# Optimization experiments

Hardware: AMD Instinct MI355X
Metric: run time of the kernel (lower is better)

Reference implementation:

```python
import jax, jax.numpy as jnp
import numpy as np

N = 131072   # total inner-graph nodes (G * n)
G = 2048     # number of inner graphs = nodes of outer graph fg
n = 64       # nodes per inner graph (contiguous blocks)
E = 1048576  # inner edges
EF = 32768   # outer (fg) edges
D = 128      # emb_dim == hidden_dim
K = 8        # SortPooling k
VOCAB = 150


def setup_inputs() -> dict:
    key = jax.random.key(0)
    ks = jax.random.split(key, 32)
    p = lambda k, shape: (jax.random.normal(k, shape, jnp.float32) * 0.1)
    inp = {
        'h': jax.random.randint(ks[0], (N,), 0, VOCAB),
        'g_src': jax.random.randint(ks[1], (E,), 0, N),
        'g_dst': jax.random.randint(ks[2], (E,), 0, N),
        'fg_src': jax.random.randint(ks[3], (EF,), 0, G),
        'fg_dst': jax.random.randint(ks[4], (EF,), 0, G),
        'token_emb': p(ks[5], (VOCAB, D)),
        # GATConv 1 (D -> D, 1 head): fc weight (in,out), attn vectors, output bias
        'W1': p(ks[6], (D, D)), 'al1': p(ks[7], (D,)), 'ar1': p(ks[8], (D,)), 'b1': p(ks[9], (D,)),
        # GATConv 2
        'W2': p(ks[10], (D, D)), 'al2': p(ks[11], (D,)), 'ar2': p(ks[12], (D,)), 'b2': p(ks[13], (D,)),
        # GATConv 3 (K*D -> D) over fg
        'W3': p(ks[14], (K * D, D)), 'al3': p(ks[15], (D,)), 'ar3': p(ks[16], (D,)), 'b3': p(ks[17], (D,)),
        # linear_forward
        'Wf': p(ks[18], (D, D)), 'bf': p(ks[19], (D,)),
        # linear
        'Wl': p(ks[20], (D, D)), 'bl': p(ks[21], (D,)),
        # linear1
        'Wl1': p(ks[22], (D, D)), 'bl1': p(ks[23], (D,)),
        # clasifier
        'Wc': p(ks[24], (D, 2)), 'bc': p(ks[25], (2,)),
    }
    return inp


def gat_conv(src, dst, num_nodes, x, W, al, ar, b):
    """DGL GATConv, num_heads=1, allow_zero_in_degree=True, no activation."""
    f = x @ W                                   # [N, D] projected features
    el = f @ al                                 # [N] left attention logits
    er = f @ ar                                 # [N] right attention logits
    e = jax.nn.leaky_relu(el[src] + er[dst], 0.2)   # [E] per-edge score
    m = jax.ops.segment_max(e, dst, num_segments=num_nodes)
    a = jnp.exp(e - m[dst])
    s = jax.ops.segment_sum(a, dst, num_segments=num_nodes)
    alpha = a / s[dst]                          # edge softmax over incoming edges
    out = jax.ops.segment_sum(alpha[:, None] * f[src], dst, num_segments=num_nodes)
    return out + b                              # zero-in-degree nodes -> bias only


def sort_pooling(x, num_graphs, nodes_per_graph, k):
    """DGL SortPooling: sort each node's feature ascending, rank nodes by last
    channel descending, take top-k, concat -> [G, k*D]."""
    d = x.shape[-1]
    x = jnp.sort(x.reshape(num_graphs, nodes_per_graph, d), axis=-1)
    idx = jnp.argsort(-x[:, :, -1], axis=1)[:, :k]          # [G, k]
    topk = jnp.take_along_axis(x, idx[:, :, None], axis=1)  # [G, k, D]
    return topk.reshape(num_graphs, k * d)


def reference(h, g_src, g_dst, fg_src, fg_dst, token_emb,
              W1, al1, ar1, b1, W2, al2, ar2, b2, W3, al3, ar3, b3,
              Wf, bf, Wl, bl, Wl1, bl1, Wc, bc):
    x = jax.nn.relu(token_emb[h])                                   # [N, D]
    x = jax.nn.relu(gat_conv(g_src, g_dst, N, x, W1, al1, ar1, b1))
    x = jax.nn.relu(gat_conv(g_src, g_dst, N, x, W2, al2, ar2, b2))
    x = jax.nn.relu(x @ Wf + bf)                                    # linear_forward
    x = sort_pooling(x, G, n, K)                                    # [G, K*D]
    x = jax.nn.relu(gat_conv(fg_src, fg_dst, G, x, W3, al3, ar3, b3))
    x = jax.nn.relu(x @ Wl + bl)                                    # dropout = eval identity
    x = jax.nn.relu(x @ Wl1 + bl1)
    x = x @ Wc + bc
    return x.reshape(-1, 2)
```

## Files before the change

kernel.cpp:

```cpp
#include <hip/hip_runtime.h>
#include <math.h>

#define NN   131072
#define GG   2048
#define NPG  64
#define EE   1048576
#define EFN  32768
#define DD   128
#define KK   8

typedef unsigned short bfu;
typedef _Float16 f16x8 __attribute__((ext_vector_type(8)));
typedef float f32x4 __attribute__((ext_vector_type(4)));

static __device__ __forceinline__ bfu f2b(float f) {
  unsigned u = __float_as_uint(f);
  u += 0x7FFFu + ((u >> 16) & 1u);
  return (bfu)(u >> 16);
}
static __device__ __forceinline__ float b2f(bfu b) {
  return __uint_as_float(((unsigned)b) << 16);
}

static __device__ __forceinline__ bfu f2h(float f) {
  _Float16 h = (_Float16)f;
  bfu u;
  __builtin_memcpy(&u, &h, 2);
  return u;
}
static __device__ __forceinline__ float h2f(bfu b) {
  _Float16 h;
  __builtin_memcpy(&h, &b, 2);
  return (float)h;
}

__global__ void fill_f32_kernel(float* __restrict__ p, float v, int nElems) {
  int i = blockIdx.x * 256 + threadIdx.x;
  if (i < nElems) p[i] = v;
}

__global__ void zero_int_kernel(int* __restrict__ p, int nElems) {
  int i = blockIdx.x * 256 + threadIdx.x;
  if (i < nElems) p[i] = 0;
}

__global__ void init_softmax_kernel(float* __restrict__ mx, float* __restrict__ sm, int nElems) {
  int i = blockIdx.x * 256 + threadIdx.x;
  if (i < nElems) { mx[i] = -INFINITY; sm[i] = 0.f; }
}

__global__ void embed_relu_kernel(const float* __restrict__ temb,
                                  const int* __restrict__ h,
                                  float* __restrict__ x, int total) {
  int i = blockIdx.x * 256 + threadIdx.x;
  if (i >= total) return;
  int node = i >> 7, d = i & 127;
  x[i] = fmaxf(temb[h[node] * DD + d], 0.f);
}

template <int KD, int ROWS>
__global__ __launch_bounds__(128) void gemm_kernel(
    const float* __restrict__ A, const float* __restrict__ W,
    const float* __restrict__ bias, float* __restrict__ out,
    int relu_flag) {
  __shared__ float As[ROWS * KD];
  const int row0 = blockIdx.x * ROWS;
  const int tid = threadIdx.x;
  for (int i = tid; i < ROWS * KD; i += 128) As[i] = A[(size_t)row0 * KD + i];
  __syncthreads();
  float acc[ROWS];
#pragma unroll
  for (int r = 0; r < ROWS; r++) acc[r] = 0.f;
  for (int k = 0; k < KD; k++) {
    float w = W[k * 128 + tid];
#pragma unroll
    for (int r = 0; r < ROWS; r++) acc[r] += As[r * KD + k] * w;
  }
  float b = bias ? bias[tid] : 0.f;
#pragma unroll
  for (int r = 0; r < ROWS; r++) {
    float v = acc[r] + b;
    if (relu_flag) v = fmaxf(v, 0.f);
    out[(size_t)(row0 + r) * 128 + tid] = v;
  }
}

__global__ __launch_bounds__(256) void gemm1024_kernel(
    const float* __restrict__ A, const float* __restrict__ W,
    float* __restrict__ out) {
  __shared__ float As[8 * 1024];
  __shared__ float red[8][256];
  const int t = threadIdx.x;
  const int row0 = blockIdx.x * 8;
  for (int idx = t; idx < 8 * 256; idx += 256) {
    int r = idx >> 8, c4 = (idx & 255) << 2;
    *(float4*)&As[r * 1024 + c4] = *(const float4*)(A + (size_t)(row0 + r) * 1024 + c4);
  }
  __syncthreads();
  const int col = t & 127, kh = t >> 7;
  const int k0 = kh * 512;
  float acc[8];
#pragma unroll
  for (int r = 0; r < 8; r++) acc[r] = 0.f;
  for (int k = k0; k < k0 + 512; k += 4) {
    float w0 = W[(size_t)(k + 0) * 128 + col];
    float w1 = W[(size_t)(k + 1) * 128 + col];
    float w2 = W[(size_t)(k + 2) * 128 + col];
    float w3 = W[(size_t)(k + 3) * 128 + col];
#pragma unroll
    for (int r = 0; r < 8; r++) {
      float4 a = *(const float4*)&As[r * 1024 + k];
      acc[r] += a.x * w0 + a.y * w1 + a.z * w2 + a.w * w3;
    }
  }
#pragma unroll
  for (int r = 0; r < 8; r++) red[r][t] = acc[r];
  __syncthreads();
  for (int idx = t; idx < 1024; idx += 256) {
    int r = idx >> 7, c = idx & 127;
    out[(size_t)(row0 + r) * 128 + c] = red[r][c] + red[r][128 + c];
  }
}

__global__ void pack_w_kernel(const float* __restrict__ W,
                              bfu* __restrict__ hi) {
  int i = blockIdx.x * 256 + threadIdx.x;
  if (i >= 16384) return;
  int k = i >> 7, n = i & 127;
  bfu h = f2h(W[i]);
  int kk = k >> 5, k5 = k & 31, quad = k5 >> 3, j = k5 & 7;
  int tt = n >> 4, m16 = n & 15;
  int pos = ((((kk * 8 + tt) * 4 + quad) * 16) + m16) * 8 + j;
  hi[pos] = h;
}

template <int SRC_MODE, int EPI>
__global__ __launch_bounds__(256) void mfma_gemm(
    const float* A, const float* __restrict__ temb,
    const int* __restrict__ hidx,
    const bfu* __restrict__ WfHi,
    const float* __restrict__ bias, void* out,
    const float* __restrict__ al, const float* __restrict__ ar,
    float* __restrict__ el, float* __restrict__ er,
    float* __restrict__ keyb) {
  const int t = threadIdx.x;
  const int lane = t & 63, wv_ = t >> 6;
  const int m16 = lane & 15, quad = lane >> 4;
  const int rowbase = blockIdx.x * 128 + wv_ * 32;
  const float* arow0 = nullptr;
  const float* arow1 = nullptr;
  const bfu* brow0 = nullptr;
  const bfu* brow1 = nullptr;
  if constexpr (SRC_MODE == 1) {
    arow0 = temb + (size_t)hidx[rowbase + m16] * 128;
    arow1 = temb + (size_t)hidx[rowbase + 16 + m16] * 128;
  } else if constexpr (SRC_MODE == 0) {
    arow0 = A + (size_t)(rowbase + m16) * 128;
    arow1 = A + (size_t)(rowbase + 16 + m16) * 128;
  } else {
    brow0 = (const bfu*)A + (size_t)(rowbase + m16) * 128;
    brow1 = (const bfu*)A + (size_t)(rowbase + 16 + m16) * 128;
  }
  f32x4 acc[2][8];
#pragma unroll
  for (int rg = 0; rg < 2; rg++)
#pragma unroll
    for (int i = 0; i < 8; i++) acc[rg][i] = (f32x4){0.f, 0.f, 0.f, 0.f};
#pragma unroll
  for (int kk = 0; kk < 4; kk++) {
    int k0 = kk * 32 + quad * 8;
    f16x8 ahi0, alo0, ahi1, alo1;
    if constexpr (SRC_MODE == 2) {
      ahi0 = *(const f16x8*)(brow0 + k0);
      ahi1 = *(const f16x8*)(brow1 + k0);
    } else {
      float av0[8], av1[8];
      *(float4*)&av0[0] = *(const float4*)(arow0 + k0);
      *(float4*)&av0[4] = *(const float4*)(arow0 + k0 + 4);
      *(float4*)&av1[0] = *(const float4*)(arow1 + k0);
      *(float4*)&av1[4] = *(const float4*)(arow1 + k0 + 4);
      if (SRC_MODE == 1) {
#pragma unroll
        for (int i = 0; i < 8; i++) {
          av0[i] = fmaxf(av0[i], 0.f);
          av1[i] = fmaxf(av1[i], 0.f);
        }
      }
#pragma unroll
      for (int i = 0; i < 8; i++) {
        _Float16 h0 = (_Float16)av0[i];
        ahi0[i] = h0;
        alo0[i] = (_Float16)(av0[i] - (float)h0);
        _Float16 h1 = (_Float16)av1[i];
        ahi1[i] = h1;
        alo1[i] = (_Float16)(av1[i] - (float)h1);
      }
    }
#pragma unroll
    for (int tt = 0; tt < 8; tt++) {
      int pos = ((((kk * 8 + tt) * 4 + quad) * 16) + m16) * 8;
      f16x8 bhi = *(const f16x8*)&WfHi[pos];
      acc[0][tt] = __builtin_amdgcn_mfma_f32_16x16x32_f16(ahi0, bhi, acc[0][tt], 0, 0, 0);
      if constexpr (SRC_MODE != 2)
        acc[0][tt] = __builtin_amdgcn_mfma_f32_16x16x32_f16(alo0, bhi, acc[0][tt], 0, 0, 0);
      acc[1][tt] = __builtin_amdgcn_mfma_f32_16x16x32_f16(ahi1, bhi, acc[1][tt], 0, 0, 0);
      if constexpr (SRC_MODE != 2)
        acc[1][tt] = __builtin_amdgcn_mfma_f32_16x16x32_f16(alo1, bhi, acc[1][tt], 0, 0, 0);
    }
  }
#pragma unroll
  for (int rg = 0; rg < 2; rg++) {
    const int rb = rowbase + rg * 16;
    if constexpr (EPI == 1) {
      float pl[4] = {0.f, 0.f, 0.f, 0.f}, pr[4] = {0.f, 0.f, 0.f, 0.f};
#pragma unroll
      for (int tt = 0; tt < 8; tt++) {
        int col = tt * 16 + m16;
        float alv = al[col], arv = ar[col];
#pragma unroll
        for (int r = 0; r < 4; r++) {
          float v = acc[rg][tt][r];
          ((bfu*)out)[(size_t)(rb + quad * 4 + r) * 128 + col] = f2h(v);
          pl[r] += v * alv;
          pr[r] += v * arv;
        }
      }
#pragma unroll
      for (int r = 0; r < 4; r++) {
        float a0 = pl[r], a1 = pr[r];
#pragma unroll
        for (int off = 1; off < 16; off <<= 1) {
          a0 += __shfl_xor(a0, off);
          a1 += __shfl_xor(a1, off);
        }
        if (m16 == 0) {
          el[rb + quad * 4 + r] = a0;
          er[rb + quad * 4 + r] = a1;
        }
      }
    } else {
      float pm[4] = {-INFINITY, -INFINITY, -INFINITY, -INFINITY};
#pragma unroll
      for (int tt = 0; tt < 8; tt++) {
        int col = tt * 16 + m16;
        float bv = bias[col];
#pragma unroll
        for (int r = 0; r < 4; r++) {
          float v = fmaxf(acc[rg][tt][r] + bv, 0.f);
          ((bfu*)out)[(size_t)(rb + quad * 4 + r) * 128 + col] = f2h(v);
          pm[r] = fmaxf(pm[r], v);
        }
      }
#pragma unroll
      for (int r = 0; r < 4; r++) {
        float a0 = pm[r];
#pragma unroll
        for (int off = 1; off < 16; off <<= 1) a0 = fmaxf(a0, __shfl_xor(a0, off));
        if (m16 == 0) keyb[rb + quad * 4 + r] = a0;
      }
    }
  }
}

__global__ __launch_bounds__(64) void attn_logits_kernel(
    const float* __restrict__ f, const float* __restrict__ al,
    const float* __restrict__ ar, float* __restrict__ el,
    float* __restrict__ er) {
  int node = blockIdx.x, lane = threadIdx.x;
  float v1 = f[(size_t)node * 128 + lane];
  float v2 = f[(size_t)node * 128 + 64 + lane];
  float sl = v1 * al[lane] + v2 * al[64 + lane];
  float sr = v1 * ar[lane] + v2 * ar[64 + lane];
#pragma unroll
  for (int off = 32; off; off >>= 1) {
    sl += __shfl_down(sl, off);
    sr += __shfl_down(sr, off);
  }
  if (lane == 0) { el[node] = sl; er[node] = sr; }
}

__global__ void hist_rank_kernel(const int* __restrict__ dst, int* __restrict__ cnt,
                                 int* __restrict__ rank, int nE) {
  int e = blockIdx.x * 256 + threadIdx.x;
  if (e < nE) rank[e] = atomicAdd(&cnt[dst[e]], 1);
}

__global__ __launch_bounds__(256) void scan_block_kernel(
    const int* __restrict__ cnt, int* __restrict__ excl, int* __restrict__ part) {
  __shared__ int s[256];
  int blk = blockIdx.x, tid = threadIdx.x;
  int base = blk * 1024 + tid * 4;
  int a0 = cnt[base], a1 = cnt[base + 1], a2 = cnt[base + 2], a3 = cnt[base + 3];
  int tsum = a0 + a1 + a2 + a3;
  s[tid] = tsum; __syncthreads();
  for (int off = 1; off < 256; off <<= 1) {
    int v = (tid >= off) ? s[tid - off] : 0;
    __syncthreads();
    s[tid] += v;
    __syncthreads();
  }
  int texcl = s[tid] - tsum;
  excl[base]     = texcl;
  excl[base + 1] = texcl + a0;
  excl[base + 2] = texcl + a0 + a1;
  excl[base + 3] = texcl + a0 + a1 + a2;
  if (tid == 255) part[blk] = s[255];
}

__global__ __launch_bounds__(128) void scan_part_kernel(int* __restrict__ part) {
  __shared__ int s[128];
  int tid = threadIdx.x;
  int orig = part[tid];
  s[tid] = orig; __syncthreads();
  for (int off = 1; off < 128; off <<= 1) {
    int v = (tid >= off) ? s[tid - off] : 0;
    __syncthreads();
    s[tid] += v;
    __syncthreads();
  }
  part[tid] = s[tid] - orig;
}

__global__ void scan_add_kernel(int* __restrict__ row_ptr, const int* __restrict__ part,
                                int n, int total) {
  int i = blockIdx.x * 256 + threadIdx.x;
  if (i < n) row_ptr[i] += part[i >> 10];
  if (i == 0) row_ptr[n] = total;
}

__global__ __launch_bounds__(256) void scan2048_kernel(const int* __restrict__ cnt,
                                                       int* __restrict__ rp, int total) {
  __shared__ int s[256];
  int t = threadIdx.x;
  int base = t * 8;
  int v[8];
  int tsum = 0;
#pragma unroll
  for (int i = 0; i < 8; i++) { v[i] = cnt[base + i]; tsum += v[i]; }
  s[t] = tsum; __syncthreads();
  for (int off = 1; off < 256; off <<= 1) {
    int x = (t >= off) ? s[t - off] : 0;
    __syncthreads();
    s[t] += x;
    __syncthreads();
  }
  int excl = s[t] - tsum;
#pragma unroll
  for (int i = 0; i < 8; i++) { rp[base + i] = excl; excl += v[i]; }
  if (t == 255) rp[2048] = total;
}

__global__ void scatter2_kernel(const int* __restrict__ dst, const int* __restrict__ src,
                                const int* __restrict__ row_ptr, const int* __restrict__ rank,
                                int* __restrict__ adj_src, int nE) {
  int e = blockIdx.x * 256 + threadIdx.x;
  if (e >= nE) return;
  adj_src[row_ptr[dst[e]] + rank[e]] = src[e];
}

__global__ __launch_bounds__(256) void gat_aggregate_csr_kernel(
    const bfu* __restrict__ F, const float* __restrict__ el,
    const float* __restrict__ er, const int* __restrict__ row_ptr,
    const int* __restrict__ adj_src,
    const float* __restrict__ bias, bfu* __restrict__ outX) {
  const int t = threadIdx.x;
  const int l = t & 31;
  const int gb = t & 32;
  const int d = blockIdx.x * 8 + (t >> 5);
  const int c0 = l * 4;
  int beg = row_ptr[d];
  int n = row_ptr[d + 1] - beg;
  float4 bv = *(const float4*)&bias[c0];
  if (n == 0) {
    ushort4 o;
    o.x = f2h(fmaxf(bv.x, 0.f)); o.y = f2h(fmaxf(bv.y, 0.f));
    o.z = f2h(fmaxf(bv.z, 0.f)); o.w = f2h(fmaxf(bv.w, 0.f));
    *(ushort4*)&outX[(size_t)d * 128 + c0] = o;
    return;
  }
  float er_d = er[d];
  float4 acc = make_float4(0.f, 0.f, 0.f, 0.f);
  if (n <= 32) {
    int sv = 0; float sc = -INFINITY;
    if (l < n) {
      sv = adj_src[beg + l];
      float v = el[sv] + er_d;
      sc = v > 0.f ? v : 0.2f * v;
    }
    float m = sc;
#pragma unroll
    for (int off = 16; off; off >>= 1) m = fmaxf(m, __shfl_xor(m, off));
    float ex = (l < n) ? expf(sc - m) : 0.f;
    float s = ex;
#pragma unroll
    for (int off = 16; off; off >>= 1) s += __shfl_xor(s, off);
    float wt = ex / s;
    for (int j = 0; j < n; j += 4) {
      int   s0 = __shfl(sv, gb + j);
      float w0 = __shfl(wt, gb + j);
      int   j1 = (j + 1 < n) ? j + 1 : j;
      int   s1 = __shfl(sv, gb + j1); float w1 = (j + 1 < n) ? __shfl(wt, gb + j1) : 0.f;
      int   j2 = (j + 2 < n) ? j + 2 : j;
      int   s2 = __shfl(sv, gb + j2); float w2 = (j + 2 < n) ? __shfl(wt, gb + j2) : 0.f;
      int   j3 = (j + 3 < n) ? j + 3 : j;
      int   s3 = __shfl(sv, gb + j3); float w3 = (j + 3 < n) ? __shfl(wt, gb + j3) : 0.f;
      ushort4 f0 = *(const ushort4*)&F[(size_t)s0 * 128 + c0];
      ushort4 f1 = *(const ushort4*)&F[(size_t)s1 * 128 + c0];
      ushort4 f2 = *(const ushort4*)&F[(size_t)s2 * 128 + c0];
      ushort4 f3 = *(const ushort4*)&F[(size_t)s3 * 128 + c0];
      acc.x += w0 * h2f(f0.x) + w1 * h2f(f1.x) + w2 * h2f(f2.x) + w3 * h2f(f3.x);
      acc.y += w0 * h2f(f0.y) + w1 * h2f(f1.y) + w2 * h2f(f2.y) + w3 * h2f(f3.y);
      acc.z += w0 * h2f(f0.z) + w1 * h2f(f1.z) + w2 * h2f(f2.z) + w3 * h2f(f3.z);
      acc.w += w0 * h2f(f0.w) + w1 * h2f(f1.w) + w2 * h2f(f2.w) + w3 * h2f(f3.w);
    }
  } else {
    float lm = -INFINITY;
    for (int e = l; e < n; e += 32) {
      int sv = adj_src[beg + e];
      float v = el[sv] + er_d;
      v = v > 0.f ? v : 0.2f * v;
      lm = fmaxf(lm, v);
    }
#pragma unroll
    for (int off = 16; off; off >>= 1) lm = fmaxf(lm, __shfl_xor(lm, off));
    float ls = 0.f;
    for (int e = l; e < n; e += 32) {
      int sv = adj_src[beg + e];
      float v = el[sv] + er_d;
      v = v > 0.f ? v : 0.2f * v;
      ls += expf(v - lm);
    }
#pragma unroll
    for (int off = 16; off; off >>= 1) ls += __shfl_xor(ls, off);
    for (int base = 0; base < n; base += 32) {
      int e = base + l;
      int sv = 0; float wt = 0.f;
      if (e < n) {
        sv = adj_src[beg + e];
        float v = el[sv] + er_d;
        v = v > 0.f ? v : 0.2f * v;
        wt = expf(v - lm) / ls;
      }
      int cnt = min(32, n - base);
      for (int j = 0; j < cnt; ++j) {
        int s0 = __shfl(sv, gb + j);
        float w0 = __shfl(wt, gb + j);
        ushort4 f0 = *(const ushort4*)&F[(size_t)s0 * 128 + c0];
        acc.x += w0 * h2f(f0.x);
        acc.y += w0 * h2f(f0.y);
        acc.z += w0 * h2f(f0.z);
        acc.w += w0 * h2f(f0.w);
      }
    }
  }
  ushort4 o;
  o.x = f2h(fmaxf(acc.x + bv.x, 0.f));
  o.y = f2h(fmaxf(acc.y + bv.y, 0.f));
  o.z = f2h(fmaxf(acc.z + bv.z, 0.f));
  o.w = f2h(fmaxf(acc.w + bv.w, 0.f));
  *(ushort4*)&outX[(size_t)d * 128 + c0] = o;
}

__global__ __launch_bounds__(256) void gat_aggregate_outer_kernel(
    const float* __restrict__ F, const float* __restrict__ el,
    const float* __restrict__ er, const int* __restrict__ row_ptr,
    const int* __restrict__ adj_src,
    const float* __restrict__ bias, float* __restrict__ outG) {
  const int t = threadIdx.x;
  const int l = t & 31;
  const int gb = t & 32;
  const int d = blockIdx.x * 8 + (t >> 5);
  const int c0 = l * 4;
  int beg = row_ptr[d];
  int n = row_ptr[d + 1] - beg;
  float4 bv = *(const float4*)&bias[c0];
  if (n == 0) {
    float4 o;
    o.x = fmaxf(bv.x, 0.f); o.y = fmaxf(bv.y, 0.f);
    o.z = fmaxf(bv.z, 0.f); o.w = fmaxf(bv.w, 0.f);
    *(float4*)&outG[(size_t)d * 128 + c0] = o;
    return;
  }
  float er_d = er[d];
  float4 acc = make_float4(0.f, 0.f, 0.f, 0.f);
  if (n <= 32) {
    int sv = 0; float sc = -INFINITY;
    if (l < n) {
      sv = adj_src[beg + l];
      float v = el[sv] + er_d;
      sc = v > 0.f ? v : 0.2f * v;
    }
    float m = sc;
#pragma unroll
    for (int off = 16; off; off >>= 1) m = fmaxf(m, __shfl_xor(m, off));
    float ex = (l < n) ? expf(sc - m) : 0.f;
    float s = ex;
#pragma unroll
    for (int off = 16; off; off >>= 1) s += __shfl_xor(s, off);
    float wt = ex / s;
    for (int j = 0; j < n; ++j) {
      int   s0 = __shfl(sv, gb + j);
      float w0 = __shfl(wt, gb + j);
      float4 f0 = *(const float4*)&F[(size_t)s0 * 128 + c0];
      acc.x += w0 * f0.x; acc.y += w0 * f0.y;
      acc.z += w0 * f0.z; acc.w += w0 * f0.w;
    }
  } else {
    float lm = -INFINITY;
    for (int e = l; e < n; e += 32) {
      int sv = adj_src[beg + e];
      float v = el[sv] + er_d;
      v = v > 0.f ? v : 0.2f * v;
      lm = fmaxf(lm, v);
    }
#pragma unroll
    for (int off = 16; off; off >>= 1) lm = fmaxf(lm, __shfl_xor(lm, off));
    float ls = 0.f;
    for (int e = l; e < n; e += 32) {
      int sv = adj_src[beg + e];
      float v = el[sv] + er_d;
      v = v > 0.f ? v : 0.2f * v;
      ls += expf(v - lm);
    }
#pragma unroll
    for (int off = 16; off; off >>= 1) ls += __shfl_xor(ls, off);
    for (int base = 0; base < n; base += 32) {
      int e = base + l;
      int sv = 0; float wt = 0.f;
      if (e < n) {
        sv = adj_src[beg + e];
        float v = el[sv] + er_d;
        v = v > 0.f ? v : 0.2f * v;
        wt = expf(v - lm) / ls;
      }
      int cnt = min(32, n - base);
      for (int j = 0; j < cnt; ++j) {
        int s0 = __shfl(sv, gb + j);
        float w0 = __shfl(wt, gb + j);
        float4 f0 = *(const float4*)&F[(size_t)s0 * 128 + c0];
        acc.x += w0 * f0.x; acc.y += w0 * f0.y;
        acc.z += w0 * f0.z; acc.w += w0 * f0.w;
      }
    }
  }
  float4 o;
  o.x = fmaxf(acc.x + bv.x, 0.f);
  o.y = fmaxf(acc.y + bv.y, 0.f);
  o.z = fmaxf(acc.z + bv.z, 0.f);
  o.w = fmaxf(acc.w + bv.w, 0.f);
  *(float4*)&outG[(size_t)d * 128 + c0] = o;
}

static __device__ __forceinline__ void atomicMaxF(float* addr, float v) {
  int iv = __float_as_int(v);
  if (iv >= 0) atomicMax((int*)addr, iv);
  else atomicMin((unsigned int*)addr, (unsigned int)iv);
}

static __device__ __forceinline__ float edge_score(const float* el, const float* er,
                                                   int sv, int dv) {
  float v = el[sv] + er[dv];
  return v > 0.f ? v : 0.2f * v;
}

__global__ void edge_max_kernel(const float* __restrict__ el,
                                const float* __restrict__ er,
                                const int* __restrict__ src,
                                const int* __restrict__ dst,
                                float* __restrict__ m, int nE) {
  int e = blockIdx.x * 256 + threadIdx.x;
  if (e >= nE) return;
  atomicMaxF(&m[dst[e]], edge_score(el, er, src[e], dst[e]));
}

__global__ void edge_expsum_kernel(const float* __restrict__ el,
                                   const float* __restrict__ er,
                                   const float* __restrict__ m,
                                   const int* __restrict__ src,
                                   const int* __restrict__ dst,
                                   float* __restrict__ s, int nE) {
  int e = blockIdx.x * 256 + threadIdx.x;
  if (e >= nE) return;
  int d = dst[e];
  atomicAdd(&s[d], expf(edge_score(el, er, src[e], d) - m[d]));
}

__global__ __launch_bounds__(128) void edge_aggregate_kernel(
    const float* __restrict__ f, const float* __restrict__ el,
    const float* __restrict__ er, const float* __restrict__ m,
    const float* __restrict__ s, const int* __restrict__ src,
    const int* __restrict__ dst, float* __restrict__ out, int nE) {
  int e = blockIdx.x;
  int d = threadIdx.x;
  int sv = src[e], dv = dst[e];
  float alpha = expf(edge_score(el, er, sv, dv) - m[dv]) / s[dv];
  atomicAdd(&out[(size_t)dv * 128 + d], alpha * f[(size_t)sv * 128 + d]);
}

__global__ void bias_relu_kernel(float* __restrict__ x,
                                 const float* __restrict__ b, int total) {
  int i = blockIdx.x * 256 + threadIdx.x;
  if (i >= total) return;
  x[i] = fmaxf(x[i] + b[i & 127], 0.f);
}

__global__ __launch_bounds__(64) void row_max_kernel(const float* __restrict__ x,
                                                     float* __restrict__ key) {
  int node = blockIdx.x, lane = threadIdx.x;
  float v = fmaxf(x[(size_t)node * 128 + lane], x[(size_t)node * 128 + 64 + lane]);
#pragma unroll
  for (int off = 32; off; off >>= 1) v = fmaxf(v, __shfl_down(v, off));
  if (lane == 0) key[node] = v;
}

__global__ __launch_bounds__(64) void select_topk_kernel(
    const float* __restrict__ key, int* __restrict__ sel) {
  __shared__ float keys[NPG];
  int g = blockIdx.x, t = threadIdx.x;
  keys[t] = key[(size_t)g * NPG + t];
  __syncthreads();
  float myk = keys[t];
  int rank = 0;
  for (int j = 0; j < NPG; ++j) {
    float kj = keys[j];
    rank += (kj > myk) || (kj == myk && j < t);
  }
  if (rank < KK) sel[g * KK + rank] = t;
}

template <int HF>
__global__ __launch_bounds__(128) void sort_rows_kernel(
    const void* __restrict__ xin, const int* __restrict__ sel,
    float* __restrict__ xp) {
  __shared__ float v[128];
  int b = blockIdx.x;
  int t = threadIdx.x;
  int g = b >> 3, r = b & 7;
  int node = sel[b];
  if (HF) v[t] = h2f(((const bfu*)xin)[(size_t)(g * NPG + node) * 128 + t]);
  else    v[t] = ((const float*)xin)[(size_t)(g * NPG + node) * 128 + t];
  __syncthreads();
  for (int k = 2; k <= 128; k <<= 1) {
    for (int j = k >> 1; j > 0; j >>= 1) {
      int ixj = t ^ j;
      if (ixj > t) {
        float a = v[t], bb = v[ixj];
        bool asc = ((t & k) == 0);
        if (asc ? (a > bb) : (a < bb)) { v[t] = bb; v[ixj] = a; }
      }
      __syncthreads();
    }
  }
  xp[(size_t)g * (KK * 128) + r * 128 + t] = v[t];
}

__global__ __launch_bounds__(128) void mlp_tail_kernel(
    const float* __restrict__ g3, const float* __restrict__ Wl,
    const float* __restrict__ bl, const float* __restrict__ Wl1,
    const float* __restrict__ bl1, const float* __restrict__ Wc,
    const float* __restrict__ bc, float* __restrict__ out) {
  __shared__ float buf[128];
  __shared__ float r0[128], r1[128];
  int g = blockIdx.x, t = threadIdx.x;
  buf[t] = g3[(size_t)g * 128 + t];
  __syncthreads();
  float a = 0.f;
  for (int k = 0; k < 128; k++) a += buf[k] * Wl[k * 128 + t];
  float t1 = fmaxf(a + bl[t], 0.f);
  __syncthreads();
  buf[t] = t1;
  __syncthreads();
  a = 0.f;
  for (int k = 0; k < 128; k++) a += buf[k] * Wl1[k * 128 + t];
  float t2 = fmaxf(a + bl1[t], 0.f);
  r0[t] = t2 * Wc[t * 2 + 0];
  r1[t] = t2 * Wc[t * 2 + 1];
  __syncthreads();
  for (int off = 64; off; off >>= 1) {
    if (t < off) { r0[t] += r0[t + off]; r1[t] += r1[t + off]; }
    __syncthreads();
  }
  if (t == 0) {
    out[g * 2 + 0] = r0[0] + bc[0];
    out[g * 2 + 1] = r1[0] + bc[1];
  }
}

extern "C" void kernel_launch(void* const* d_in, const int* in_sizes, int n_in,
                              void* d_out, int out_size, void* d_ws, size_t ws_size,
                              hipStream_t stream) {
  const size_t BASE_FLOATS = (size_t)NN * DD * 2 + (size_t)NN * 4;
  const size_t CSR_INTS = (size_t)(NN + 1) + NN + EE + 128;
  if (ws_size < BASE_FLOATS * sizeof(float)) {
    hipMemsetAsync(d_out, 0, (size_t)out_size * sizeof(float), stream);
    return;
  }
  const bool use_csr = ws_size >= BASE_FLOATS * sizeof(float) + CSR_INTS * sizeof(int);

  const int* h      = (const int*)d_in[0];
  const int* g_src  = (const int*)d_in[1];
  const int* g_dst  = (const int*)d_in[2];
  const int* fg_src = (const int*)d_in[3];
  const int* fg_dst = (const int*)d_in[4];
  const float* temb = (const float*)d_in[5];
  const float* W1 = (const float*)d_in[6];
  const float* al1 = (const float*)d_in[7];
  const float* ar1 = (const float*)d_in[8];
  const float* b1 = (const float*)d_in[9];
  const float* W2 = (const float*)d_in[10];
  const float* al2 = (const float*)d_in[11];
  const float* ar2 = (const float*)d_in[12];
  const float* b2 = (const float*)d_in[13];
  const float* W3 = (const float*)d_in[14];
  const float* al3 = (const float*)d_in[15];
  const float* ar3 = (const float*)d_in[16];
  const float* b3 = (const float*)d_in[17];
  const float* Wf = (const float*)d_in[18];
  const float* bfv = (const float*)d_in[19];
  const float* Wl = (const float*)d_in[20];
  const float* bl = (const float*)d_in[21];
  const float* Wl1 = (const float*)d_in[22];
  const float* bl1 = (const float*)d_in[23];
  const float* Wc = (const float*)d_in[24];
  const float* bc = (const float*)d_in[25];
  float* out = (float*)d_out;

  float* ws = (float*)d_ws;
  float* X  = ws;
  float* F  = X + (size_t)NN * DD;
  float* el = F + (size_t)NN * DD;
  float* er = el + NN;
  float* mx = er + NN;
  float* sm = mx + NN;
  int* row_ptr = (int*)(sm + NN);
  int* cursor  = row_ptr + NN + 1;
  int* adj_src = cursor + NN;
  int* part    = adj_src + EE;
  int* rankb = (int*)X;
  bfu* w1h = (bfu*)mx;
  bfu* w2h = w1h + 16384;
  bfu* wfh = w2h + 16384;
  int* ocnt  = (int*)X;
  int* orp   = ocnt + 2048;
  int* orank = orp + 2080;
  int* oadj  = orank + EFN;
  float* xp   = F;
  float* f3   = F + 2097152;
  float* g3   = f3 + (size_t)GG * DD;
  float* t1   = g3 + (size_t)GG * DD;
  float* t2   = t1 + (size_t)GG * DD;
  float* keyb = t2 + (size_t)GG * DD;
  int*   sel  = (int*)(keyb + NN);

  const int totalND = NN * DD;

  if (use_csr) {
    bfu* Fb = (bfu*)F;
    bfu* Xb = (bfu*)X;
    zero_int_kernel<<<NN / 256, 256, 0, stream>>>(cursor, NN);
    hist_rank_kernel<<<EE / 256, 256, 0, stream>>>(g_dst, cursor, rankb, EE);
    scan_block_kernel<<<NN / 1024, 256, 0, stream>>>(cursor, row_ptr, part);
    scan_part_kernel<<<1, 128, 0, stream>>>(part);
    scan_add_kernel<<<(NN + 255) / 256, 256, 0, stream>>>(row_ptr, part, NN, EE);
    scatter2_kernel<<<EE / 256, 256, 0, stream>>>(g_dst, g_src, row_ptr, rankb, adj_src, EE);

    pack_w_kernel<<<64, 256, 0, stream>>>(W1, w1h);
    pack_w_kernel<<<64, 256, 0, stream>>>(W2, w2h);
    pack_w_kernel<<<64, 256, 0, stream>>>(Wf, wfh);

    mfma_gemm<1, 1><<<NN / 128, 256, 0, stream>>>(
        nullptr, temb, h, w1h, nullptr, Fb, al1, ar1, el, er, nullptr);
    gat_aggregate_csr_kernel<<<NN / 8, 256, 0, stream>>>(Fb, el, er, row_ptr, adj_src, b1, Xb);

    mfma_gemm<2, 1><<<NN / 128, 256, 0, stream>>>(
        (const float*)X, nullptr, nullptr, w2h, nullptr, Fb, al2, ar2, el, er, nullptr);
    gat_aggregate_csr_kernel<<<NN / 8, 256, 0, stream>>>(Fb, el, er, row_ptr, adj_src, b2, Xb);

    mfma_gemm<2, 2><<<NN / 128, 256, 0, stream>>>(
        (const float*)X, nullptr, nullptr, wfh, bfv, Xb, nullptr, nullptr, nullptr, nullptr, keyb);

    select_topk_kernel<<<GG, 64, 0, stream>>>(keyb, sel);
    sort_rows_kernel<1><<<GG * KK, 128, 0, stream>>>(Xb, sel, xp);

    gemm1024_kernel<<<GG / 8, 256, 0, stream>>>(xp, W3, f3);
    attn_logits_kernel<<<GG, 64, 0, stream>>>(f3, al3, ar3, el, er);
    zero_int_kernel<<<GG / 256, 256, 0, stream>>>(ocnt, GG);
    hist_rank_kernel<<<EFN / 256, 256, 0, stream>>>(fg_dst, ocnt, orank, EFN);
    scan2048_kernel<<<1, 256, 0, stream>>>(ocnt, orp, EFN);
    scatter2_kernel<<<EFN / 256, 256, 0, stream>>>(fg_dst, fg_src, orp, orank, oadj, EFN);
    gat_aggregate_outer_kernel<<<GG / 8, 256, 0, stream>>>(f3, el, er, orp, oadj, b3, g3);

    mlp_tail_kernel<<<GG, 128, 0, stream>>>(g3, Wl, bl, Wl1, bl1, Wc, bc, out);
  } else {
    embed_relu_kernel<<<totalND / 256, 256, 0, stream>>>(temb, h, X, totalND);
    auto gat_inner = [&](const float* W, const float* al, const float* ar, const float* bb) {
      gemm_kernel<DD, 8><<<NN / 8, 128, 0, stream>>>(X, W, nullptr, F, 0);
      attn_logits_kernel<<<NN, 64, 0, stream>>>(F, al, ar, el, er);
      init_softmax_kernel<<<(NN + 255) / 256, 256, 0, stream>>>(mx, sm, NN);
      fill_f32_kernel<<<totalND / 256, 256, 0, stream>>>(X, 0.f, totalND);
      edge_max_kernel<<<(EE + 255) / 256, 256, 0, stream>>>(el, er, g_src, g_dst, mx, EE);
      edge_expsum_kernel<<<(EE + 255) / 256, 256, 0, stream>>>(el, er, mx, g_src, g_dst, sm, EE);
      edge_aggregate_kernel<<<EE, 128, 0, stream>>>(F, el, er, mx, sm, g_src, g_dst, X, EE);
      bias_relu_kernel<<<totalND / 256, 256, 0, stream>>>(X, bb, totalND);
    };
    gat_inner(W1, al1, ar1, b1);
    gat_inner(W2, al2, ar2, b2);
    gemm_kernel<DD, 8><<<NN / 8, 128, 0, stream>>>(X, Wf, bfv, X, 1);
    row_max_kernel<<<NN, 64, 0, stream>>>(X, keyb);

    select_topk_kernel<<<GG, 64, 0, stream>>>(keyb, sel);
    sort_rows_kernel<0><<<GG * KK, 128, 0, stream>>>(X, sel, xp);

    gemm1024_kernel<<<GG / 8, 256, 0, stream>>>(xp, W3, f3);
    attn_logits_kernel<<<GG, 64, 0, stream>>>(f3, al3, ar3, el, er);
    init_softmax_kernel<<<(GG + 255) / 256, 256, 0, stream>>>(mx, sm, GG);
    fill_f32_kernel<<<(GG * DD + 255) / 256, 256, 0, stream>>>(g3, 0.f, GG * DD);
    edge_max_kernel<<<(EFN + 255) / 256, 256, 0, stream>>>(el, er, fg_src, fg_dst, mx, EFN);
    edge_expsum_kernel<<<(EFN + 255) / 256, 256, 0, stream>>>(el, er, mx, fg_src, fg_dst, sm, EFN);
    edge_aggregate_kernel<<<EFN, 128, 0, stream>>>(f3, el, er, mx, sm, fg_src, fg_dst, g3, EFN);
    bias_relu_kernel<<<(GG * DD + 255) / 256, 256, 0, stream>>>(g3, b3, GG * DD);
    mlp_tail_kernel<<<GG, 128, 0, stream>>>(g3, Wl, bl, Wl1, bl1, Wc, bc, out);
  }
}
```

Baseline: 458.8 us.

## Precompute layer-1 GAT projection per vocab token and fuse top-k, outer CSR, logits

Layer 1's input is relu(token_emb[h]), so the projection and attention logits are computed once per vocabulary entry (150 rows) rather than for all 131072 nodes. The aggregation then gathers projected features by token id, which removes the first large MFMA GEMM. The change also merges top-k selection with the row sort into one kernel and folds the outer-graph attention logits into the 1024-wide GEMM epilogue. The outer CSR build becomes a single-block kernel, which trades a few launches for serial work on one CU and an extra h[] indirection per edge.

```diff
diff --git a/kernel.cpp b/kernel.cpp
--- a/kernel.cpp
+++ b/kernel.cpp
@@ -8,6 +8,7 @@
 #define EFN  32768
 #define DD   128
 #define KK   8
+#define VOCAB 150
 
 typedef unsigned short bfu;
 typedef _Float16 f16x8 __attribute__((ext_vector_type(8)));
@@ -85,9 +86,33 @@
   }
 }
 
+__global__ __launch_bounds__(128) void vocab_l1_kernel(
+    const float* __restrict__ temb, const float* __restrict__ W1,
+    const float* __restrict__ al1, const float* __restrict__ ar1,
+    bfu* __restrict__ fvh, float* __restrict__ elv, float* __restrict__ erv) {
+  __shared__ float xs[128];
+  __shared__ float rl[128], rr[128];
+  int v = blockIdx.x, t = threadIdx.x;
+  xs[t] = fmaxf(temb[v * 128 + t], 0.f);
+  __syncthreads();
+  float acc = 0.f;
+  for (int k = 0; k < 128; k++) acc += xs[k] * W1[k * 128 + t];
+  fvh[v * 128 + t] = f2h(acc);
+  rl[t] = acc * al1[t];
+  rr[t] = acc * ar1[t];
+  __syncthreads();
+  for (int off = 64; off; off >>= 1) {
+    if (t < off) { rl[t] += rl[t + off]; rr[t] += rr[t + off]; }
+    __syncthreads();
+  }
+  if (t == 0) { elv[v] = rl[0]; erv[v] = rr[0]; }
+}
+
 __global__ __launch_bounds__(256) void gemm1024_kernel(
     const float* __restrict__ A, const float* __restrict__ W,
-    float* __restrict__ out) {
+    float* __restrict__ out,
+    const float* __restrict__ al, const float* __restrict__ ar,
+    float* __restrict__ el, float* __restrict__ er) {
   __shared__ float As[8 * 1024];
   __shared__ float red[8][256];
   const int t = threadIdx.x;
@@ -118,27 +143,42 @@
   __syncthreads();
   for (int idx = t; idx < 1024; idx += 256) {
     int r = idx >> 7, c = idx & 127;
-    out[(size_t)(row0 + r) * 128 + c] = red[r][c] + red[r][128 + c];
-  }
-}
-
-__global__ void pack_w_kernel(const float* __restrict__ W,
-                              bfu* __restrict__ hi) {
+    float val = red[r][c] + red[r][128 + c];
+    out[(size_t)(row0 + r) * 128 + c] = val;
+    As[idx] = val * al[c];
+    As[4096 + idx] = val * ar[c];
+  }
+  __syncthreads();
+  if (t < 8) {
+    float s = 0.f;
+    for (int c = 0; c < 128; c++) s += As[t * 128 + c];
+    el[row0 + t] = s;
+  } else if (t < 16) {
+    int r = t - 8;
+    float s = 0.f;
+    for (int c = 0; c < 128; c++) s += As[4096 + r * 128 + c];
+    er[row0 + r] = s;
+  }
+}
+
+__global__ void pack_w2_kernel(const float* __restrict__ W2, const float* __restrict__ Wf,
+                               bfu* __restrict__ w2h, bfu* __restrict__ wfh) {
   int i = blockIdx.x * 256 + threadIdx.x;
-  if (i >= 16384) return;
-  int k = i >> 7, n = i & 127;
-  bfu h = f2h(W[i]);
+  if (i >= 32768) return;
+  const float* W = (i < 16384) ? W2 : Wf;
+  bfu* dst = (i < 16384) ? w2h : wfh;
+  int ii = i & 16383;
+  int k = ii >> 7, n = ii & 127;
+  bfu h = f2h(W[ii]);
   int kk = k >> 5, k5 = k & 31, quad = k5 >> 3, j = k5 & 7;
   int tt = n >> 4, m16 = n & 15;
   int pos = ((((kk * 8 + tt) * 4 + quad) * 16) + m16) * 8 + j;
-  hi[pos] = h;
+  dst[pos] = h;
 }
 
 template <int SRC_MODE, int EPI>
 __global__ __launch_bounds__(256) void mfma_gemm(
-    const float* A, const float* __restrict__ temb,
-    const int* __restrict__ hidx,
-    const bfu* __restrict__ WfHi,
+    const float* A, const bfu* __restrict__ WfHi,
     const float* __restrict__ bias, void* out,
     const float* __restrict__ al, const float* __restrict__ ar,
     float* __restrict__ el, float* __restrict__ er,
@@ -151,10 +191,7 @@
   const float* arow1 = nullptr;
   const bfu* brow0 = nullptr;
   const bfu* brow1 = nullptr;
-  if constexpr (SRC_MODE == 1) {
-    arow0 = temb + (size_t)hidx[rowbase + m16] * 128;
-    arow1 = temb + (size_t)hidx[rowbase + 16 + m16] * 128;
-  } else if constexpr (SRC_MODE == 0) {
+  if constexpr (SRC_MODE == 0) {
     arow0 = A + (size_t)(rowbase + m16) * 128;
     arow1 = A + (size_t)(rowbase + 16 + m16) * 128;
   } else {
@@ -179,13 +216,6 @@
       *(float4*)&av0[4] = *(const float4*)(arow0 + k0 + 4);
       *(float4*)&av1[0] = *(const float4*)(arow1 + k0);
       *(float4*)&av1[4] = *(const float4*)(arow1 + k0 + 4);
-      if (SRC_MODE == 1) {
-#pragma unroll
-        for (int i = 0; i < 8; i++) {
-          av0[i] = fmaxf(av0[i], 0.f);
-          av1[i] = fmaxf(av1[i], 0.f);
-        }
-      }
 #pragma unroll
       for (int i = 0; i < 8; i++) {
         _Float16 h0 = (_Float16)av0[i];
@@ -328,34 +358,147 @@
   if (i == 0) row_ptr[n] = total;
 }
 
-__global__ __launch_bounds__(256) void scan2048_kernel(const int* __restrict__ cnt,
-                                                       int* __restrict__ rp, int total) {
-  __shared__ int s[256];
-  int t = threadIdx.x;
-  int base = t * 8;
-  int v[8];
-  int tsum = 0;
-#pragma unroll
-  for (int i = 0; i < 8; i++) { v[i] = cnt[base + i]; tsum += v[i]; }
-  s[t] = tsum; __syncthreads();
-  for (int off = 1; off < 256; off <<= 1) {
-    int x = (t >= off) ? s[t - off] : 0;
-    __syncthreads();
-    s[t] += x;
-    __syncthreads();
-  }
-  int excl = s[t] - tsum;
-#pragma unroll
-  for (int i = 0; i < 8; i++) { rp[base + i] = excl; excl += v[i]; }
-  if (t == 255) rp[2048] = total;
-}
-
 __global__ void scatter2_kernel(const int* __restrict__ dst, const int* __restrict__ src,
                                 const int* __restrict__ row_ptr, const int* __restrict__ rank,
                                 int* __restrict__ adj_src, int nE) {
   int e = blockIdx.x * 256 + threadIdx.x;
   if (e >= nE) return;
   adj_src[row_ptr[dst[e]] + rank[e]] = src[e];
+}
+
+__global__ __launch_bounds__(1024) void outer_csr_kernel(
+    const int* __restrict__ fg_dst, const int* __restrict__ fg_src,
+    int* __restrict__ orp, int* __restrict__ oadj) {
+  __shared__ int cnt[2048];
+  __shared__ int ssum[1024];
+  __shared__ int cur[2048];
+  int t = threadIdx.x;
+  cnt[t] = 0; cnt[t + 1024] = 0;
+  __syncthreads();
+  for (int e = t; e < EFN; e += 1024) atomicAdd(&cnt[fg_dst[e]], 1);
+  __syncthreads();
+  int a0 = cnt[2 * t], a1 = cnt[2 * t + 1];
+  int tsum = a0 + a1;
+  ssum[t] = tsum; __syncthreads();
+  for (int off = 1; off < 1024; off <<= 1) {
+    int v = (t >= off) ? ssum[t - off] : 0;
+    __syncthreads();
+    ssum[t] += v;
+    __syncthreads();
+  }
+  int excl = ssum[t] - tsum;
+  orp[2 * t] = excl;       cur[2 * t] = excl;
+  orp[2 * t + 1] = excl + a0; cur[2 * t + 1] = excl + a0;
+  if (t == 1023) orp[2048] = EFN;
+  __syncthreads();
+  for (int e = t; e < EFN; e += 1024) {
+    int d = fg_dst[e];
+    int slot = atomicAdd(&cur[d], 1);
+    oadj[slot] = fg_src[e];
+  }
+}
+
+__global__ __launch_bounds__(256) void gat_aggregate_vocab_kernel(
+    const bfu* __restrict__ fvh, const float* __restrict__ elv,
+    const float* __restrict__ erv, const int* __restrict__ h,
+    const int* __restrict__ row_ptr, const int* __restrict__ adj_src,
+    const float* __restrict__ bias, bfu* __restrict__ outX) {
+  const int t = threadIdx.x;
+  const int l = t & 31;
+  const int gb = t & 32;
+  const int d = blockIdx.x * 8 + (t >> 5);
+  const int c0 = l * 4;
+  int beg = row_ptr[d];
+  int n = row_ptr[d + 1] - beg;
+  float4 bv = *(const float4*)&bias[c0];
+  if (n == 0) {
+    ushort4 o;
+    o.x = f2h(fmaxf(bv.x, 0.f)); o.y = f2h(fmaxf(bv.y, 0.f));
+    o.z = f2h(fmaxf(bv.z, 0.f)); o.w = f2h(fmaxf(bv.w, 0.f));
+    *(ushort4*)&outX[(size_t)d * 128 + c0] = o;
+    return;
+  }
+  float er_d = erv[h[d]];
+  float4 acc = make_float4(0.f, 0.f, 0.f, 0.f);
+  if (n <= 32) {
+    int hv = 0; float sc = -INFINITY;
+    if (l < n) {
+      hv = h[adj_src[beg + l]];
+      float v = elv[hv] + er_d;
+      sc = v > 0.f ? v : 0.2f * v;
+    }
+    float m = sc;
+#pragma unroll
+    for (int off = 16; off; off >>= 1) m = fmaxf(m, __shfl_xor(m, off));
+    float ex = (l < n) ? expf(sc - m) : 0.f;
+    float s = ex;
+#pragma unroll
+    for (int off = 16; off; off >>= 1) s += __shfl_xor(s, off);
+    float wt = ex / s;
+    for (int j = 0; j < n; j += 4) {
+      int   h0 = __shfl(hv, gb + j);
+      float w0 = __shfl(wt, gb + j);
+      int   j1 = (j + 1 < n) ? j + 1 : j;
+      int   h1 = __shfl(hv, gb + j1); float w1 = (j + 1 < n) ? __shfl(wt, gb + j1) : 0.f;
+      int   j2 = (j + 2 < n) ? j + 2 : j;
+      int   h2 = __shfl(hv, gb + j2); float w2 = (j + 2 < n) ? __shfl(wt, gb + j2) : 0.f;
+      int   j3 = (j + 3 < n) ? j + 3 : j;
+      int   h3 = __shfl(hv, gb + j3); float w3 = (j + 3 < n) ? __shfl(wt, gb + j3) : 0.f;
+      ushort4 f0 = *(const ushort4*)&fvh[(size_t)h0 * 128 + c0];
+      ushort4 f1 = *(const ushort4*)&fvh[(size_t)h1 * 128 + c0];
+      ushort4 f2 = *(const ushort4*)&fvh[(size_t)h2 * 128 + c0];
+      ushort4 f3 = *(const ushort4*)&fvh[(size_t)h3 * 128 + c0];
+      acc.x += w0 * h2f(f0.x) + w1 * h2f(f1.x) + w2 * h2f(f2.x) + w3 * h2f(f3.x);
+      acc.y += w0 * h2f(f0.y) + w1 * h2f(f1.y) + w2 * h2f(f2.y) + w3 * h2f(f3.y);
+      acc.z += w0 * h2f(f0.z) + w1 * h2f(f1.z) + w2 * h2f(f2.z) + w3 * h2f(f3.z);
+      acc.w += w0 * h2f(f0.w) + w1 * h2f(f1.w) + w2 * h2f(f2.w) + w3 * h2f(f3.w);
+    }
+  } else {
+    float lm = -INFINITY;
+    for (int e = l; e < n; e += 32) {
+      int hv = h[adj_src[beg + e]];
+      float v = elv[hv] + er_d;
+      v = v > 0.f ? v : 0.2f * v;
+      lm = fmaxf(lm, v);
+    }
+#pragma unroll
+    for (int off = 16; off; off >>= 1) lm = fmaxf(lm, __shfl_xor(lm, off));
+    float ls = 0.f;
+    for (int e = l; e < n; e += 32) {
+      int hv = h[adj_src[beg + e]];
+      float v = elv[hv] + er_d;
+      v = v > 0.f ? v : 0.2f * v;
+      ls += expf(v - lm);
+    }
+#pragma unroll
+    for (int off = 16; off; off >>= 1) ls += __shfl_xor(ls, off);
+    for (int base = 0; base < n; base += 32) {
+      int e = base + l;
+      int hv = 0; float wt = 0.f;
+      if (e < n) {
+        hv = h[adj_src[beg + e]];
+        float v = elv[hv] + er_d;
+        v = v > 0.f ? v : 0.2f * v;
+        wt = expf(v - lm) / ls;
+      }
+      int cnt = min(32, n - base);
+      for (int j = 0; j < cnt; ++j) {
+        int h0 = __shfl(hv, gb + j);
+        float w0 = __shfl(wt, gb + j);
+        ushort4 f0 = *(const ushort4*)&fvh[(size_t)h0 * 128 + c0];
+        acc.x += w0 * h2f(f0.x);
+        acc.y += w0 * h2f(f0.y);
+        acc.z += w0 * h2f(f0.z);
+        acc.w += w0 * h2f(f0.w);
+      }
+    }
+  }
+  ushort4 o;
+  o.x = f2h(fmaxf(acc.x + bv.x, 0.f));
+  o.y = f2h(fmaxf(acc.y + bv.y, 0.f));
+  o.z = f2h(fmaxf(acc.z + bv.z, 0.f));
+  o.w = f2h(fmaxf(acc.w + bv.w, 0.f));
+  *(ushort4*)&outX[(size_t)d * 128 + c0] = o;
 }
 
 __global__ __launch_bounds__(256) void gat_aggregate_csr_kernel(
@@ -626,6 +769,43 @@
     rank += (kj > myk) || (kj == myk && j < t);
   }
   if (rank < KK) sel[g * KK + rank] = t;
+}
+
+__global__ __launch_bounds__(1024) void topk_sort_kernel(
+    const float* __restrict__ keyb, const bfu* __restrict__ xin,
+    float* __restrict__ xp) {
+  __shared__ float keys[NPG];
+  __shared__ int sel_l[KK];
+  __shared__ float v[1024];
+  int g = blockIdx.x, t = threadIdx.x;
+  if (t < NPG) keys[t] = keyb[(size_t)g * NPG + t];
+  __syncthreads();
+  if (t < NPG) {
+    float myk = keys[t];
+    int rank = 0;
+    for (int j = 0; j < NPG; ++j) {
+      float kj = keys[j];
+      rank += (kj > myk) || (kj == myk && j < t);
+    }
+    if (rank < KK) sel_l[rank] = t;
+  }
+  __syncthreads();
+  int r = t >> 7, c = t & 127;
+  int node = sel_l[r];
+  v[t] = h2f(xin[(size_t)(g * NPG + node) * 128 + c]);
+  __syncthreads();
+  for (int k = 2; k <= 128; k <<= 1) {
+    for (int j = k >> 1; j > 0; j >>= 1) {
+      int ixj = c ^ j;
+      if (ixj > c) {
+        float a = v[r * 128 + c], bb = v[r * 128 + ixj];
+        bool asc = ((c & k) == 0);
+        if (asc ? (a > bb) : (a < bb)) { v[r * 128 + c] = bb; v[r * 128 + ixj] = a; }
+      }
+      __syncthreads();
+    }
+  }
+  xp[(size_t)g * 1024 + t] = v[t];
 }
 
 template <int HF>
@@ -737,9 +917,11 @@
   int* adj_src = cursor + NN;
   int* part    = adj_src + EE;
   int* rankb = (int*)X;
-  bfu* w1h = (bfu*)mx;
-  bfu* w2h = w1h + 16384;
+  bfu* w2h = (bfu*)mx;
   bfu* wfh = w2h + 16384;
+  bfu* fvh = wfh + 16384;
+  float* elv = (float*)(fvh + VOCAB * 128 + 128);
+  float* erv = elv + VOCAB;
   int* ocnt  = (int*)X;
   int* orp   = ocnt + 2048;
   int* orank = orp + 2080;
@@ -764,30 +946,23 @@
     scan_add_kernel<<<(NN + 255) / 256, 256, 0, stream>>>(row_ptr, part, NN, EE);
     scatter2_kernel<<<EE / 256, 256, 0, stream>>>(g_dst, g_src, row_ptr, rankb, adj_src, EE);
 
-    pack_w_kernel<<<64, 256, 0, stream>>>(W1, w1h);
-    pack_w_kernel<<<64, 256, 0, stream>>>(W2, w2h);
-    pack_w_kernel<<<64, 256, 0, stream>>>(Wf, wfh);
-
-    mfma_gemm<1, 1><<<NN / 128, 256, 0, stream>>>(
-        nullptr, temb, h, w1h, nullptr, Fb, al1, ar1, el, er, nullptr);
-    gat_aggregate_csr_kernel<<<NN / 8, 256, 0, stream>>>(Fb, el, er, row_ptr, adj_src, b1, Xb);
+    pack_w2_kernel<<<128, 256, 0, stream>>>(W2, Wf, w2h, wfh);
+    vocab_l1_kernel<<<VOCAB, 128, 0, stream>>>(temb, W1, al1, ar1, fvh, elv, erv);
+
+    gat_aggregate_vocab_kernel<<<NN / 8, 256, 0, stream>>>(
+        fvh, elv, erv, h, row_ptr, adj_src, b1, Xb);
 
     mfma_gemm<2, 1><<<NN / 128, 256, 0, stream>>>(
-        (const float*)X, nullptr, nullptr, w2h, nullptr, Fb, al2, ar2, el, er, nullptr);
+        (const float*)X, w2h, nullptr, Fb, al2, ar2, el, er, nullptr);
     gat_aggregate_csr_kernel<<<NN / 8, 256, 0, stream>>>(Fb, el, er, row_ptr, adj_src, b2, Xb);
 
     mfma_gemm<2, 2><<<NN / 128, 256, 0, stream>>>(
-        (const float*)X, nullptr, nullptr, wfh, bfv, Xb, nullptr, nullptr, nullptr, nullptr, keyb);
-
-    select_topk_kernel<<<GG, 64, 0, stream>>>(keyb, sel);
-    sort_rows_kernel<1><<<GG * KK, 128, 0, stream>>>(Xb, sel, xp);
-
-    gemm1024_kernel<<<GG / 8, 256, 0, stream>>>(xp, W3, f3);
-    attn_logits_kernel<<<GG, 64, 0, stream>>>(f3, al3, ar3, el, er);
-    zero_int_kernel<<<GG / 256, 256, 0, stream>>>(ocnt, GG);
-    hist_rank_kernel<<<EFN / 256, 256, 0, stream>>>(fg_dst, ocnt, orank, EFN);
-    scan2048_kernel<<<1, 256, 0, stream>>>(ocnt, orp, EFN);
-    scatter2_kernel<<<EFN / 256, 256, 0, stream>>>(fg_dst, fg_src, orp, orank, oadj, EFN);
+        (const float*)X, wfh, bfv, Xb, nullptr, nullptr, nullptr, nullptr, keyb);
+
+    topk_sort_kernel<<<GG, 1024, 0, stream>>>(keyb, Xb, xp);
+
+    gemm1024_kernel<<<GG / 8, 256, 0, stream>>>(xp, W3, f3, al3, ar3, el, er);
+    outer_csr_kernel<<<1, 1024, 0, stream>>>(fg_dst, fg_src, orp, oadj);
     gat_aggregate_outer_kernel<<<GG / 8, 256, 0, stream>>>(f3, el, er, orp, oadj, b3, g3);
 
     mlp_tail_kernel<<<GG, 128, 0, stream>>>(g3, Wl, bl, Wl1, bl1, Wc, bc, out);
@@ -811,8 +986,7 @@
     select_topk_kernel<<<GG, 64, 0, stream>>>(keyb, sel);
     sort_rows_kernel<0><<<GG * KK, 128, 0, stream>>>(X, sel, xp);
 
-    gemm1024_kernel<<<GG / 8, 256, 0, stream>>>(xp, W3, f3);
-    attn_logits_kernel<<<GG, 64, 0, stream>>>(f3, al3, ar3, el, er);
+    gemm1024_kernel<<<GG / 8, 256, 0, stream>>>(xp, W3, f3, al3, ar3, el, er);
     init_softmax_kernel<<<(GG + 255) / 256, 256, 0, stream>>>(mx, sm, GG);
     fill_f32_kernel<<<(GG * DD + 255) / 256, 256, 0, stream>>>(g3, 0.f, GG * DD);
     edge_max_kernel<<<(EFN + 255) / 256, 256, 0, stream>>>(el, er, fg_src, fg_dst, mx, EFN);
```

New measurement: 451.2 us. No clear change (-1.7%).
